# Optimization experiments

Hardware: AMD Instinct MI355X
Metric: run time of the kernel (lower is better)

## Reference

```python
import jax, jax.numpy as jnp
import numpy as np

B, S, D, H = 2, 2048, 1024, 16
HD = D // H  # head_dim = 64


def setup_inputs() -> dict:
    key = jax.random.key(0)
    ks = jax.random.split(key, 6)
    scale = 0.02
    return {
        "x": jax.random.normal(ks[0], (B, S, D), dtype=jnp.float32),
        "wq": jax.random.normal(ks[1], (D, D), dtype=jnp.float32) * scale,  # torch Linear weight [out,in]
        "wk": jax.random.normal(ks[2], (D, D), dtype=jnp.float32) * scale,
        "wv": jax.random.normal(ks[3], (D, D), dtype=jnp.float32) * scale,
        "wo": jax.random.normal(ks[4], (D, D), dtype=jnp.float32) * scale,
        "bo": jnp.zeros((D,), dtype=jnp.float32),
    }


def reference(x, wq, wk, wv, wo, bo):
    b, t, d = x.shape
    # projections (torch nn.Linear: x @ W.T), split into heads -> [b, h, t, hd]
    def split_heads(y):
        return y.reshape(b, t, H, HD).transpose(0, 2, 1, 3)

    q = split_heads(x @ wq.T)
    k = split_heads(x @ wk.T)
    v = split_heads(x @ wv.T)

    scores = jnp.einsum("bhqd,bhkd->bhqk", q, k)  # [b,h,t,t]
    causal = jnp.triu(jnp.ones((t, t), dtype=bool), k=1)
    scores = jnp.where(causal, -jnp.inf, scores)
    attn = jax.nn.softmax(scores / jnp.sqrt(jnp.asarray(HD, scores.dtype)), axis=-1)
    # dropout p=0.0 -> identity (eval-mode reference)
    ctx = jnp.einsum("bhqk,bhkd->bhqd", attn, v)
    ctx = ctx.transpose(0, 2, 1, 3).reshape(b, t, d)
    return ctx @ wo.T + bo
```

## Files before the change

### kernel.cpp

```cpp
#include <hip/hip_runtime.h>
#include <hip/hip_bf16.h>
#include <stdint.h>
#include <math.h>

#define NH   16
#define HDIM 64
#define SEQ  2048
#define DM   1024
#define NB   2
#define MTOK (NB * SEQ)

typedef __bf16 bf16x8 __attribute__((ext_vector_type(8)));
typedef __bf16 bf16x4 __attribute__((ext_vector_type(4)));
typedef short  short4v __attribute__((ext_vector_type(4)));
typedef float  f32x4  __attribute__((ext_vector_type(4)));

__device__ __forceinline__ unsigned short f2bf(float f) {
  union { float f; unsigned int u; } c; c.f = f;
  unsigned int u = c.u;
  return (unsigned short)((u + 0x7FFFu + ((u >> 16) & 1u)) >> 16);
}
__device__ __forceinline__ float bf2f(unsigned short s) {
  union { unsigned int u; float f; } c; c.u = ((unsigned int)s) << 16;
  return c.f;
}
__device__ __forceinline__ unsigned int pk2bf(float a, float b) {
  __hip_bfloat162 h = __float22bfloat162_rn(float2{a, b});
  return *reinterpret_cast<unsigned int*>(&h);
}

__device__ __forceinline__ f32x4 mfma16(short4v a, short4v b, f32x4 c) {
#if __has_builtin(__builtin_amdgcn_mfma_f32_16x16x16_bf16)
  return __builtin_amdgcn_mfma_f32_16x16x16_bf16(
      __builtin_bit_cast(bf16x4, a), __builtin_bit_cast(bf16x4, b), c, 0, 0, 0);
#else
  return __builtin_amdgcn_mfma_f32_16x16x16bf16_1k(a, b, c, 0, 0, 0);
#endif
}

__device__ __forceinline__ void async_copy16(const void* g, void* l) {
  __builtin_amdgcn_global_load_lds((__attribute__((address_space(1))) void*)g,
                                   (__attribute__((address_space(3))) void*)l,
                                   16, 0, 0);
}

__global__ void cast_all(const float* __restrict__ x,  const float* __restrict__ wq,
                         const float* __restrict__ wk, const float* __restrict__ wv,
                         const float* __restrict__ wo,
                         unsigned short* __restrict__ xb,
                         unsigned short* __restrict__ wqkvb,
                         unsigned short* __restrict__ wob) {
  const int i = blockIdx.x * 256 + threadIdx.x;
  float4 v;
  uint2* dstp;
  int idx;
  if (i < (1 << 20)) {
    v = reinterpret_cast<const float4*>(x)[i];
    dstp = reinterpret_cast<uint2*>(xb); idx = i;
  } else {
    const int j = i - (1 << 20);
    const int seg = j >> 18;
    idx = j & ((1 << 18) - 1);
    const float* w = (seg == 0) ? wq : (seg == 1) ? wk : (seg == 2) ? wv : wo;
    v = reinterpret_cast<const float4*>(w)[idx];
    if (seg < 3) { dstp = reinterpret_cast<uint2*>(wqkvb); idx += seg * (1 << 18); }
    else         { dstp = reinterpret_cast<uint2*>(wob); }
  }
  uint2 o;
  o.x = pk2bf(v.x, v.y); o.y = pk2bf(v.z, v.w);
  dstp[idx] = o;
}

#define QSCALE 0.1803368801111244f
template <int MODE>
__global__ __launch_bounds__(256, 2) void gemm_bt(
    const unsigned short* __restrict__ A,
    const unsigned short* __restrict__ B,
    unsigned short* __restrict__ qo, unsigned short* __restrict__ ko,
    unsigned short* __restrict__ vo,
    float* __restrict__ co, const float* __restrict__ bias,
    int M, int N, int K) {
  constexpr int BN = (MODE == 0) ? 128 : 64;
  constexpr int TJ = BN / 32;
  constexpr int RB = BN * 4 / 256;
  __shared__ __align__(16) unsigned short As[128 * 32];
  __shared__ __align__(16) unsigned short Bs[BN * 32];

  const int tid  = threadIdx.x;
  const int lane = tid & 63;
  const int wave = tid >> 6;
  const int l15  = lane & 15;
  const int quad = lane >> 4;
  const int wm   = (wave >> 1) * 64;
  const int wn   = (wave & 1) * (BN / 2);
  const int m0   = blockIdx.x * 128;
  const int n0   = blockIdx.y * BN;

  f32x4 acc[4][TJ];
#pragma unroll
  for (int a = 0; a < 4; ++a)
#pragma unroll
    for (int b = 0; b < TJ; ++b) acc[a][b] = f32x4{0.f, 0.f, 0.f, 0.f};

  for (int k0 = 0; k0 < K; k0 += 32) {
    __syncthreads();
#pragma unroll
    for (int s = 0; s < 2; ++s) {
      const int c   = tid + s * 256;
      const int row = c >> 2;
      const int col = (c & 3) * 8;
      unsigned short* lA = As + ((size_t)wave * 64 + s * 256) * 8;
      async_copy16(A + (size_t)(m0 + row) * K + k0 + col, lA);
    }
#pragma unroll
    for (int s = 0; s < RB; ++s) {
      const int c   = tid + s * 256;
      const int row = c >> 2;
      const int col = (c & 3) * 8;
      unsigned short* lB = Bs + ((size_t)wave * 64 + s * 256) * 8;
      async_copy16(B + (size_t)(n0 + row) * K + k0 + col, lB);
    }
    __syncthreads();

    bf16x8 af[4], bfr[TJ];
#pragma unroll
    for (int t = 0; t < 4; ++t)
      af[t]  = *reinterpret_cast<const bf16x8*>(As + (wm + t * 16 + l15) * 32 + quad * 8);
#pragma unroll
    for (int t = 0; t < TJ; ++t)
      bfr[t] = *reinterpret_cast<const bf16x8*>(Bs + (wn + t * 16 + l15) * 32 + quad * 8);
#pragma unroll
    for (int ti = 0; ti < 4; ++ti)
#pragma unroll
      for (int tj = 0; tj < TJ; ++tj)
        acc[ti][tj] = __builtin_amdgcn_mfma_f32_16x16x32_bf16(af[ti], bfr[tj], acc[ti][tj], 0, 0, 0);
  }

#pragma unroll
  for (int ti = 0; ti < 4; ++ti) {
#pragma unroll
    for (int tj = 0; tj < TJ; ++tj) {
      const int mb = m0 + wm + ti * 16 + quad * 4;
      const int n  = n0 + wn + tj * 16 + l15;
      if (MODE == 0) {
        const int which = n >> 10;
        const int n1 = n & 1023;
        const int h = n1 >> 6, d = n1 & 63;
        const int b = mb >> 11, s = mb & 2047;
        if (which == 0) {
          const size_t idx = ((size_t)(b * NH + h) * SEQ + s) * HDIM + d;
#pragma unroll
          for (int r = 0; r < 4; ++r) qo[idx + (size_t)r * HDIM] = f2bf(acc[ti][tj][r] * QSCALE);
        } else if (which == 1) {
          const size_t idx = ((size_t)(b * NH + h) * SEQ + s) * HDIM + d;
#pragma unroll
          for (int r = 0; r < 4; ++r) ko[idx + (size_t)r * HDIM] = f2bf(acc[ti][tj][r]);
        } else {
          const size_t idx = ((size_t)(b * NH + h) * HDIM + d) * SEQ + s;
          uint2 pk;
          pk.x = pk2bf(acc[ti][tj][0], acc[ti][tj][1]);
          pk.y = pk2bf(acc[ti][tj][2], acc[ti][tj][3]);
          *reinterpret_cast<uint2*>(vo + idx) = pk;
        }
      } else {
#pragma unroll
        for (int r = 0; r < 4; ++r)
          co[(size_t)(mb + r) * N + n] = acc[ti][tj][r] + bias[n];
      }
    }
  }
}

#define KST 72

__global__ __launch_bounds__(256, 6) void flash_attn_mfma(
    const unsigned short* __restrict__ Qb,
    const unsigned short* __restrict__ Kb,
    const unsigned short* __restrict__ Vtg,
    unsigned short* __restrict__ ctx,
    unsigned short* __restrict__ pO,
    float* __restrict__ pL) {
  __shared__ __align__(16) unsigned short Ks[64 * KST];
  __shared__ __align__(16) unsigned short Vt[64 * KST];

  const int tid  = threadIdx.x;
  const int bh   = blockIdx.y;
  const int lane = tid & 63;
  const int wave = tid >> 6;
  const int l15  = lane & 15;
  const int quad = lane >> 4;

  int qt, chunk, nch;
  {
    const int x = blockIdx.x;
    if (x < 12)      { qt = x;                 chunk = 0;            nch = 1; }
    else if (x < 36) { qt = 12 + (x - 12) / 2; chunk = (x - 12) % 2; nch = 2; }
    else             { qt = 24 + (x - 36) / 3; chunk = (x - 36) % 3; nch = 3; }
  }
  const int q0 = qt * 64;
  const int c0 = chunk * 12;
  const int c1 = min(qt, c0 + 11);

  const size_t baseQK = (size_t)bh * SEQ * HDIM;
  const size_t baseV  = (size_t)bh * HDIM * SEQ;

  const int srow = tid >> 3;
  const int scol = (tid & 7) * 8;

  bf16x8 qf[2];
  {
    const unsigned short* qp = Qb + baseQK + (size_t)(q0 + wave * 16 + l15) * HDIM + quad * 8;
    qf[0] = *reinterpret_cast<const bf16x8*>(qp);
    qf[1] = *reinterpret_cast<const bf16x8*>(qp + 32);
  }

  float l_acc = 0.f;
  f32x4 o[4];
#pragma unroll
  for (int td = 0; td < 4; ++td) o[td] = f32x4{0.f, 0.f, 0.f, 0.f};

  for (int kt = c0; kt <= c1; ++kt) {
    __syncthreads();
    {
      const uint4 k0v = *reinterpret_cast<const uint4*>(Kb + baseQK + (size_t)(kt * 64 + srow) * HDIM + scol);
      const uint4 k1v = *reinterpret_cast<const uint4*>(Kb + baseQK + (size_t)(kt * 64 + srow + 32) * HDIM + scol);
      const uint4 v0v = *reinterpret_cast<const uint4*>(Vtg + baseV + (size_t)srow * SEQ + kt * 64 + scol);
      const uint4 v1v = *reinterpret_cast<const uint4*>(Vtg + baseV + (size_t)(srow + 32) * SEQ + kt * 64 + scol);
      *reinterpret_cast<uint4*>(&Ks[srow * KST + scol]) = k0v;
      *reinterpret_cast<uint4*>(&Ks[(srow + 32) * KST + scol]) = k1v;
      *reinterpret_cast<uint4*>(&Vt[srow * KST + scol]) = v0v;
      *reinterpret_cast<uint4*>(&Vt[(srow + 32) * KST + scol]) = v1v;
    }
    __syncthreads();

    const int tmax = (kt == qt) ? wave : 3;

#pragma unroll
    for (int t = 0; t < 4; ++t) {
      if (t <= tmax) {
        f32x4 c = f32x4{0.f, 0.f, 0.f, 0.f};
        const int krow = (t * 16 + l15) * KST;
        const bf16x8 kf0 = *reinterpret_cast<const bf16x8*>(&Ks[krow + quad * 8]);
        const bf16x8 kf1 = *reinterpret_cast<const bf16x8*>(&Ks[krow + 32 + quad * 8]);
        c = __builtin_amdgcn_mfma_f32_16x16x32_bf16(kf0, qf[0], c, 0, 0, 0);
        c = __builtin_amdgcn_mfma_f32_16x16x32_bf16(kf1, qf[1], c, 0, 0, 0);
        if (kt == qt && t == wave) {
#pragma unroll
          for (int r = 0; r < 4; ++r)
            if (quad * 4 + r > l15) c[r] = -INFINITY;
        }

        const float p0 = exp2f(c[0]);
        const float p1 = exp2f(c[1]);
        const float p2 = exp2f(c[2]);
        const float p3 = exp2f(c[3]);
        l_acc += (p0 + p1) + (p2 + p3);
        union { uint2 u; short4v s; } pf;
        pf.u.x = pk2bf(p0, p1);
        pf.u.y = pk2bf(p2, p3);

#pragma unroll
        for (int td = 0; td < 4; ++td) {
          const short4v vf = *reinterpret_cast<const short4v*>(
              &Vt[(td * 16 + l15) * KST + t * 16 + quad * 4]);
          o[td] = mfma16(pf.s, vf, o[td]);
        }
      }
    }
  }

  float l_s = l_acc;
  l_s += __shfl_xor(l_s, 16, 64);
  l_s += __shfl_xor(l_s, 32, 64);

  if (nch == 1) {
    const float linv = 1.f / l_s;
    const int b = bh >> 4, h = bh & 15;
#pragma unroll
    for (int r = 0; r < 4; ++r) {
      const float lr = __shfl(linv, quad * 4 + r, 64);
      const int sr = q0 + wave * 16 + quad * 4 + r;
      const size_t ob = (size_t)(b * SEQ + sr) * DM + h * HDIM + l15;
#pragma unroll
      for (int td = 0; td < 4; ++td)
        ctx[ob + td * 16] = f2bf(o[td][r] * lr);
    }
  } else {
    const int pb = (qt < 24) ? 2 * (qt - 12) : 24 + 3 * (qt - 24);
    const int pidx = bh * 48 + pb + chunk;
    if (quad == 0) pL[pidx * 64 + wave * 16 + l15] = l_s;
    unsigned short* po = pO + (size_t)pidx * 4096;
#pragma unroll
    for (int r = 0; r < 4; ++r) {
      const int ql = wave * 16 + quad * 4 + r;
#pragma unroll
      for (int td = 0; td < 4; ++td)
        po[ql * 64 + td * 16 + l15] = f2bf(o[td][r]);
    }
  }
}

__global__ __launch_bounds__(256, 8) void attn_reduce(
    const unsigned short* __restrict__ pO, const float* __restrict__ pL,
    unsigned short* __restrict__ ctx) {
  const int x = blockIdx.x;
  int qt, pb, nch;
  if (x < 12) { qt = 12 + x; pb = 2 * x;            nch = 2; }
  else        { qt = 24 + (x - 12); pb = 24 + 3 * (x - 12); nch = 3; }
  const int bh = blockIdx.y;
  const int b = bh >> 4, h = bh & 15;
  const int pidx = bh * 48 + pb;

  const int tid = threadIdx.x;
  const int ql  = tid >> 2;
  const int d0  = (tid & 3) * 16;

  float acc[16];
#pragma unroll
  for (int e = 0; e < 16; ++e) acc[e] = 0.f;
  float lsum = 0.f;

  for (int c = 0; c < nch; ++c) {
    lsum += pL[(pidx + c) * 64 + ql];
    const unsigned short* src = pO + (size_t)(pidx + c) * 4096 + ql * 64 + d0;
    const uint4 v0 = *reinterpret_cast<const uint4*>(src);
    const uint4 v1 = *reinterpret_cast<const uint4*>(src + 8);
    const unsigned short* u = reinterpret_cast<const unsigned short*>(&v0);
    const unsigned short* w = reinterpret_cast<const unsigned short*>(&v1);
#pragma unroll
    for (int e = 0; e < 8; ++e) { acc[e] += bf2f(u[e]); acc[8 + e] += bf2f(w[e]); }
  }

  const float linv = 1.f / lsum;
  unsigned int outw[8];
#pragma unroll
  for (int e = 0; e < 8; ++e)
    outw[e] = pk2bf(acc[2 * e] * linv, acc[2 * e + 1] * linv);
  unsigned short* dst = ctx + (size_t)(b * SEQ + qt * 64 + ql) * DM + h * HDIM + d0;
  *reinterpret_cast<uint4*>(dst)     = *reinterpret_cast<uint4*>(&outw[0]);
  *reinterpret_cast<uint4*>(dst + 8) = *reinterpret_cast<uint4*>(&outw[4]);
}

extern "C" void kernel_launch(void* const* d_in, const int* in_sizes, int n_in,
                              void* d_out, int out_size, void* d_ws, size_t ws_size,
                              hipStream_t stream) {
  const float* x  = (const float*)d_in[0];
  const float* wq = (const float*)d_in[1];
  const float* wk = (const float*)d_in[2];
  const float* wv = (const float*)d_in[3];
  const float* wo = (const float*)d_in[4];
  const float* bo = (const float*)d_in[5];
  float* out = (float*)d_out;

  char* ws = (char*)d_ws;
  unsigned short* xb    = (unsigned short*)(ws);
  unsigned short* wqkvb = (unsigned short*)(ws + (8ull  << 20));
  unsigned short* wob   = (unsigned short*)(ws + (14ull << 20));
  unsigned short* Qb    = (unsigned short*)(ws + (16ull << 20));
  unsigned short* Kb    = (unsigned short*)(ws + (24ull << 20));
  unsigned short* Vtg   = (unsigned short*)(ws + (32ull << 20));
  unsigned short* ctxb  = (unsigned short*)(ws + (40ull << 20));
  unsigned short* pO    = (unsigned short*)(ws);
  float*          pL    = (float*)(ws + (12ull << 20));

  cast_all<<<8192, 256, 0, stream>>>(x, wq, wk, wv, wo, xb, wqkvb, wob);

  dim3 g1(MTOK / 128, (3 * DM) / 128);
  gemm_bt<0><<<g1, 256, 0, stream>>>(xb, wqkvb, Qb, Kb, Vtg, nullptr, nullptr,
                                     MTOK, 3 * DM, DM);

  dim3 g2(60, NB * NH);
  flash_attn_mfma<<<g2, 256, 0, stream>>>(Qb, Kb, Vtg, ctxb, pO, pL);

  dim3 gr(20, NB * NH);
  attn_reduce<<<gr, 256, 0, stream>>>(pO, pL, ctxb);

  dim3 g3(MTOK / 128, DM / 64);
  gemm_bt<1><<<g3, 256, 0, stream>>>(ctxb, wob, nullptr, nullptr, nullptr, out, bo,
                                     MTOK, DM, DM);
}
```

Before: 187.7 us.

## Double-buffer K/V tiles with async LDS copies and XOR swizzle in flash attention

The attention kernel now stages K and V tiles into two LDS buffers using asynchronous global-to-LDS copies. The next tile is prefetched while the current one is computed, and one barrier per iteration replaces the previous load-then-barrier sequence. The padded row stride is replaced by an XOR column swizzle to avoid LDS bank conflicts without padding. Launch bounds are also changed: the projection GEMM goes up to 3 blocks and attention drops to 5. This hides load latency at the cost of doubled shared memory and correctness that depends on async-copy completion being waited on before the barrier.

```diff
diff --git a/kernel.cpp b/kernel.cpp
--- a/kernel.cpp
+++ b/kernel.cpp
@@ -73,7 +73,7 @@
 
 #define QSCALE 0.1803368801111244f
 template <int MODE>
-__global__ __launch_bounds__(256, 2) void gemm_bt(
+__global__ __launch_bounds__(256, 3) void gemm_bt(
     const unsigned short* __restrict__ A,
     const unsigned short* __restrict__ B,
     unsigned short* __restrict__ qo, unsigned short* __restrict__ ko,
@@ -171,17 +171,15 @@
   }
 }
 
-#define KST 72
-
-__global__ __launch_bounds__(256, 6) void flash_attn_mfma(
+__global__ __launch_bounds__(256, 5) void flash_attn_mfma(
     const unsigned short* __restrict__ Qb,
     const unsigned short* __restrict__ Kb,
     const unsigned short* __restrict__ Vtg,
     unsigned short* __restrict__ ctx,
     unsigned short* __restrict__ pO,
     float* __restrict__ pL) {
-  __shared__ __align__(16) unsigned short Ks[64 * KST];
-  __shared__ __align__(16) unsigned short Vt[64 * KST];
+  __shared__ __align__(16) unsigned short Ks[2][64 * 64];
+  __shared__ __align__(16) unsigned short Vt[2][64 * 64];
 
   const int tid  = threadIdx.x;
   const int bh   = blockIdx.y;
@@ -189,6 +187,7 @@
   const int wave = tid >> 6;
   const int l15  = lane & 15;
   const int quad = lane >> 4;
+  const int sw   = l15 & 7;
 
   int qt, chunk, nch;
   {
@@ -204,8 +203,20 @@
   const size_t baseQK = (size_t)bh * SEQ * HDIM;
   const size_t baseV  = (size_t)bh * HDIM * SEQ;
 
-  const int srow = tid >> 3;
-  const int scol = (tid & 7) * 8;
+  const unsigned short* kptr[2];
+  const unsigned short* vptr[2];
+  unsigned short* ldst = nullptr;
+  int ldsc[2];
+#pragma unroll
+  for (int s = 0; s < 2; ++s) {
+    const int P   = s * 256 + tid;
+    const int row = P >> 3;
+    const int cc  = ((P & 7) ^ (row & 7)) * 8;
+    kptr[s] = Kb + baseQK + (size_t)(c0 * 64 + row) * HDIM + cc;
+    vptr[s] = Vtg + baseV + (size_t)row * SEQ + c0 * 64 + cc;
+    ldsc[s] = (s * 256 + wave * 64) * 8;
+  }
+  (void)ldst;
 
   bf16x8 qf[2];
   {
@@ -219,19 +230,27 @@
 #pragma unroll
   for (int td = 0; td < 4; ++td) o[td] = f32x4{0.f, 0.f, 0.f, 0.f};
 
+#pragma unroll
+  for (int s = 0; s < 2; ++s) {
+    async_copy16(kptr[s], &Ks[0][ldsc[s]]);
+    async_copy16(vptr[s], &Vt[0][ldsc[s]]);
+    kptr[s] += 64 * HDIM;
+    vptr[s] += 64;
+  }
+
   for (int kt = c0; kt <= c1; ++kt) {
+    const int buf = (kt - c0) & 1;
     __syncthreads();
-    {
-      const uint4 k0v = *reinterpret_cast<const uint4*>(Kb + baseQK + (size_t)(kt * 64 + srow) * HDIM + scol);
-      const uint4 k1v = *reinterpret_cast<const uint4*>(Kb + baseQK + (size_t)(kt * 64 + srow + 32) * HDIM + scol);
-      const uint4 v0v = *reinterpret_cast<const uint4*>(Vtg + baseV + (size_t)srow * SEQ + kt * 64 + scol);
-      const uint4 v1v = *reinterpret_cast<const uint4*>(Vtg + baseV + (size_t)(srow + 32) * SEQ + kt * 64 + scol);
-      *reinterpret_cast<uint4*>(&Ks[srow * KST + scol]) = k0v;
-      *reinterpret_cast<uint4*>(&Ks[(srow + 32) * KST + scol]) = k1v;
-      *reinterpret_cast<uint4*>(&Vt[srow * KST + scol]) = v0v;
-      *reinterpret_cast<uint4*>(&Vt[(srow + 32) * KST + scol]) = v1v;
-    }
-    __syncthreads();
+
+    if (kt < c1) {
+#pragma unroll
+      for (int s = 0; s < 2; ++s) {
+        async_copy16(kptr[s], &Ks[buf ^ 1][ldsc[s]]);
+        async_copy16(vptr[s], &Vt[buf ^ 1][ldsc[s]]);
+        kptr[s] += 64 * HDIM;
+        vptr[s] += 64;
+      }
+    }
 
     const int tmax = (kt == qt) ? wave : 3;
 
@@ -239,9 +258,9 @@
     for (int t = 0; t < 4; ++t) {
       if (t <= tmax) {
         f32x4 c = f32x4{0.f, 0.f, 0.f, 0.f};
-        const int krow = (t * 16 + l15) * KST;
-        const bf16x8 kf0 = *reinterpret_cast<const bf16x8*>(&Ks[krow + quad * 8]);
-        const bf16x8 kf1 = *reinterpret_cast<const bf16x8*>(&Ks[krow + 32 + quad * 8]);
+        const int krow = (t * 16 + l15) * 64;
+        const bf16x8 kf0 = *reinterpret_cast<const bf16x8*>(&Ks[buf][krow + (quad ^ sw) * 8]);
+        const bf16x8 kf1 = *reinterpret_cast<const bf16x8*>(&Ks[buf][krow + ((4 + quad) ^ sw) * 8]);
         c = __builtin_amdgcn_mfma_f32_16x16x32_bf16(kf0, qf[0], c, 0, 0, 0);
         c = __builtin_amdgcn_mfma_f32_16x16x32_bf16(kf1, qf[1], c, 0, 0, 0);
         if (kt == qt && t == wave) {
@@ -259,10 +278,12 @@
         pf.u.x = pk2bf(p0, p1);
         pf.u.y = pk2bf(p2, p3);
 
+        const int lc = 2 * t + (quad >> 1);
+        const int vcol = ((lc ^ sw) * 8) + (quad & 1) * 4;
 #pragma unroll
         for (int td = 0; td < 4; ++td) {
           const short4v vf = *reinterpret_cast<const short4v*>(
-              &Vt[(td * 16 + l15) * KST + t * 16 + quad * 4]);
+              &Vt[buf][(td * 16 + l15) * 64 + vcol]);
           o[td] = mfma16(pf.s, vf, o[td]);
         }
       }
```

After: 195.1 us. 3.9% more time.
